# Kernel tuning notes

Hardware: AMD Instinct MI355X
Metric: run time of the kernel (lower is better)

The kernel has to match this reference:

```python
import jax, jax.numpy as jnp
import numpy as np

B, S, D, H, HD = 2, 2048, 1024, 16, 64
DFF = 4 * D
EPS = 1e-6


def _rms(x, w):
    return w * (x * jax.lax.rsqrt(jnp.mean(x * x, axis=-1, keepdims=True) + EPS))


def _rope(x, rope):
    # x: [B, H, S, HD], rope: [S, HD, 2]
    cos = rope[..., 0][None, None]
    sin = rope[..., 1][None, None]
    xr = x.reshape(*x.shape[:-1], -1, 2)
    rot = jnp.stack([-xr[..., 1], xr[..., 0]], axis=-1).reshape(x.shape)
    return x * cos + rot * sin


def setup_inputs() -> dict:
    key = jax.random.key(0)
    ks = jax.random.split(key, 10)
    w = lambda k, shape: jax.random.normal(k, shape, jnp.float32) * 0.02
    return {
        "hidden_states": jax.random.normal(ks[0], (B, S, D), jnp.float32),
        "timestep": jax.random.normal(ks[1], (B, D), jnp.float32),
        "rope_pos_embed": jax.random.normal(ks[2], (S, HD, 2), jnp.float32),
        "adaln_w": w(ks[3], (6 * D, D)),
        "adaln_b": jnp.zeros((6 * D,), jnp.float32),
        "wq": w(ks[4], (D, D)),
        "wk": w(ks[5], (D, D)),
        "wv": w(ks[6], (D, D)),
        "wo": w(ks[7], (D, D)),
        "q_norm_w": jnp.ones((D,), jnp.float32),
        "k_norm_w": jnp.ones((D,), jnp.float32),
        "norm3_w": jnp.ones((D,), jnp.float32),
        "fc1_w": w(ks[8], (DFF, D)),
        "fc1_b": jnp.zeros((DFF,), jnp.float32),
        "fc2_w": w(ks[9], (D, DFF)),
        "fc2_b": jnp.zeros((D,), jnp.float32),
    }


def reference(hidden_states, timestep, rope_pos_embed, adaln_w, adaln_b,
              wq, wk, wv, wo, q_norm_w, k_norm_w, norm3_w,
              fc1_w, fc1_b, fc2_w, fc2_b):
    x = hidden_states  # [B, S, D]
    # AdaLayerNorm: emb = Linear(SiLU(timestep)) -> 6 modulation chunks, broadcast over seq
    emb = jax.nn.silu(timestep) @ adaln_w.T + adaln_b  # [B, 6D]
    sh_msa, sc_msa, g_msa, sh_mlp, sc_mlp, g_mlp = jnp.split(emb[:, None, :], 6, axis=-1)
    mu = jnp.mean(x, axis=-1, keepdims=True)
    var = jnp.mean((x - mu) ** 2, axis=-1, keepdims=True)
    ln = (x - mu) * jax.lax.rsqrt(var + EPS)
    xm = ln * (1.0 + sc_msa) + sh_msa  # modulated input to attention

    # Attention: projections + RMSNorm over inner_dim + RoPE + SDPA
    q = _rms(xm @ wq.T, q_norm_w)
    k = _rms(xm @ wk.T, k_norm_w)
    v = xm @ wv.T
    q = q.reshape(B, S, H, HD).transpose(0, 2, 1, 3)
    k = k.reshape(B, S, H, HD).transpose(0, 2, 1, 3)
    v = v.reshape(B, S, H, HD).transpose(0, 2, 1, 3)
    q = _rope(q, rope_pos_embed)
    k = _rope(k, rope_pos_embed)
    scores = jnp.einsum('bhqd,bhkd->bhqk', q, k) * (HD ** -0.5)
    attn = jax.nn.softmax(scores, axis=-1)
    o = jnp.einsum('bhqk,bhkd->bhqd', attn, v)
    o = o.transpose(0, 2, 1, 3).reshape(B, S, H * HD) @ wo.T

    h = x + g_msa * o  # gated residual

    # MLP branch with AdaLN scale/shift on RMSNorm output
    n3 = _rms(h, norm3_w)
    nm = n3 * (1.0 + sc_mlp) + sh_mlp
    ff = jax.nn.gelu(nm @ fc1_w.T + fc1_b, approximate=True) @ fc2_w.T + fc2_b
    return h + g_mlp * ff
```

## Files before the change

kernel.cpp:

```cpp
#include <hip/hip_runtime.h>
#include <cstdint>
#include <cstddef>

typedef unsigned short ushort_t;
typedef __attribute__((ext_vector_type(8))) short s8v;
typedef __attribute__((ext_vector_type(4))) short s4v;
typedef __attribute__((ext_vector_type(4))) float f4v;

#define MFMA16(a, b, c) __builtin_amdgcn_mfma_f32_16x16x32_bf16(a, b, c, 0, 0, 0)

__device__ __forceinline__ ushort_t f2bf(float f) {
  union { float f; unsigned u; } a; a.f = f;
  return (ushort_t)((a.u + 0x7fffu + ((a.u >> 16) & 1u)) >> 16);
}
__device__ __forceinline__ float bf2f(ushort_t h) {
  union { unsigned u; float f; } a; a.u = ((unsigned)h) << 16; return a.f;
}
__device__ __forceinline__ unsigned fbits(float f) {
  union { float f; unsigned u; } a; a.f = f; return a.u;
}

__device__ __forceinline__ void gload16(const void* g, void* l) {
  __builtin_amdgcn_global_load_lds(
      (__attribute__((address_space(1))) void*)(uintptr_t)g,
      (__attribute__((address_space(3))) void*)(unsigned)(uintptr_t)l,
      16, 0, 0);
}

__launch_bounds__(256)
__global__ void convert_w(const float* __restrict__ wq, const float* __restrict__ wk,
                          const float* __restrict__ wv, const float* __restrict__ wo,
                          const float* __restrict__ f1, const float* __restrict__ f2,
                          ushort_t* __restrict__ dqkv, ushort_t* __restrict__ dwo,
                          ushort_t* __restrict__ df1, ushort_t* __restrict__ df2)
{
  const int blk = blockIdx.x;
  const float* src; ushort_t* dst; int off;
  if      (blk < 1024) { src = wq; dst = dqkv;            off = blk; }
  else if (blk < 2048) { src = wk; dst = dqkv + 1048576;  off = blk - 1024; }
  else if (blk < 3072) { src = wv; dst = dqkv + 2097152;  off = blk - 2048; }
  else if (blk < 4096) { src = wo; dst = dwo;             off = blk - 3072; }
  else if (blk < 8192) { src = f1; dst = df1;             off = blk - 4096; }
  else                 { src = f2; dst = df2;             off = blk - 8192; }
  const int idx = off * 1024 + threadIdx.x * 4;
  float4 v = *(const float4*)(src + idx);
  s4v o;
  o[0] = (short)f2bf(v.x); o[1] = (short)f2bf(v.y);
  o[2] = (short)f2bf(v.z); o[3] = (short)f2bf(v.w);
  *(s4v*)(dst + idx) = o;
}

__launch_bounds__(256)
__global__ void adaln(const float* __restrict__ ts, const float* __restrict__ w,
                      const float* __restrict__ bias, float* __restrict__ emb)
{
  const int j = blockIdx.x * 4 + (threadIdx.x >> 6);
  const int lane = threadIdx.x & 63;
  const float* wr = w + (size_t)j * 1024;
  float s0 = 0.f, s1 = 0.f;
  for (int i = lane; i < 1024; i += 64) {
    const float wv = wr[i];
    const float t0 = ts[i], t1 = ts[1024 + i];
    const float e0 = __builtin_amdgcn_exp2f(-1.4426950409f * t0);
    const float e1 = __builtin_amdgcn_exp2f(-1.4426950409f * t1);
    s0 += wv * t0 * __builtin_amdgcn_rcpf(1.f + e0);
    s1 += wv * t1 * __builtin_amdgcn_rcpf(1.f + e1);
  }
  #pragma unroll
  for (int m = 32; m; m >>= 1) { s0 += __shfl_down(s0, m); s1 += __shfl_down(s1, m); }
  if (!lane) { emb[j] = s0 + bias[j]; emb[6144 + j] = s1 + bias[j]; }
}

__launch_bounds__(256)
__global__ void ln_mod(const float* __restrict__ x, const float* __restrict__ emb,
                       ushort_t* __restrict__ xm)
{
  const int row = blockIdx.x, b = row >> 11, tid = threadIdx.x;
  const float* xr = x + (size_t)row * 1024;
  const int c = tid * 4;
  float4 v = *(const float4*)(xr + c);
  float s  = v.x + v.y + v.z + v.w;
  float s2 = v.x*v.x + v.y*v.y + v.z*v.z + v.w*v.w;
  #pragma unroll
  for (int m = 32; m; m >>= 1) { s += __shfl_down(s, m); s2 += __shfl_down(s2, m); }
  __shared__ float red[8];
  const int wave = tid >> 6, lane = tid & 63;
  if (!lane) { red[wave] = s; red[4 + wave] = s2; }
  __syncthreads();
  const float mu = (red[0] + red[1] + red[2] + red[3]) * (1.f / 1024.f);
  const float ms = (red[4] + red[5] + red[6] + red[7]) * (1.f / 1024.f);
  const float rstd = rsqrtf(ms - mu * mu + 1e-6f);
  const float* sh = emb + b * 6144;
  const float* sc = emb + b * 6144 + 1024;
  float4 shv = *(const float4*)(sh + c);
  float4 scv = *(const float4*)(sc + c);
  s4v ov;
  ov[0] = (short)f2bf((v.x - mu) * rstd * (1.f + scv.x) + shv.x);
  ov[1] = (short)f2bf((v.y - mu) * rstd * (1.f + scv.y) + shv.y);
  ov[2] = (short)f2bf((v.z - mu) * rstd * (1.f + scv.z) + shv.z);
  ov[3] = (short)f2bf((v.w - mu) * rstd * (1.f + scv.w) + shv.w);
  *(s4v*)(xm + (size_t)row * 1024 + c) = ov;
}

template<int EPI, int TN>
__launch_bounds__(256, 4)
__global__ void gemm_bt(const ushort_t* __restrict__ A, const ushort_t* __restrict__ Bw,
                        int K, int N,
                        ushort_t* __restrict__ outb, float* __restrict__ outf,
                        const float* __restrict__ bias, const float* __restrict__ resid,
                        const float* __restrict__ emb, int gate_off)
{
  constexpr int JN = TN / 32;
  constexpr int BUFB = TN * 32;
  __shared__ ushort_t As0[128 * 32], As1[128 * 32];
  __shared__ ushort_t Bs0[BUFB],    Bs1[BUFB];
  const int tid = threadIdx.x;
  const int wave = tid >> 6, lane = tid & 63;
  const int quad = lane >> 4, r = lane & 15;
  const int m0 = blockIdx.y * 128, n0 = blockIdx.x * TN;
  const int wm = (wave >> 1) * 64, wn = (wave & 1) * (TN / 2);

  const int srow = wave * 16 + (lane >> 2);
  const int scol = (lane & 3) * 8;
  const ushort_t* ag = A  + (size_t)(m0 + srow) * K + scol;
  const ushort_t* bg = Bw + (size_t)(n0 + srow) * K + scol;
  const size_t rowK64 = (size_t)64 * K;

  f4v acc[4][JN] = {};

  auto stage = [&](ushort_t* as, ushort_t* bs) {
    gload16(ag,          as + wave * 512);
    gload16(ag + rowK64, as + wave * 512 + 2048);
    gload16(bg,          bs + wave * 512);
    if (TN == 128) gload16(bg + rowK64, bs + wave * 512 + 2048);
    ag += 32; bg += 32;
  };
  auto compute = [&](const ushort_t* ab, const ushort_t* bb) {
    s8v af[4], bf[JN];
    #pragma unroll
    for (int i = 0; i < 4; i++)
      af[i] = *(const s8v*)(ab + (wm + i * 16 + r) * 32 + quad * 8);
    #pragma unroll
    for (int j = 0; j < JN; j++)
      bf[j] = *(const s8v*)(bb + (wn + j * 16 + r) * 32 + quad * 8);
    #pragma unroll
    for (int i = 0; i < 4; i++)
      #pragma unroll
      for (int j = 0; j < JN; j++)
        acc[i][j] = MFMA16(af[i], bf[j], acc[i][j]);
  };

  stage(As0, Bs0);
  __syncthreads();
  const int R = (K >> 6) - 1;
  for (int it = 0; it < R; it++) {
    stage(As1, Bs1);
    compute(As0, Bs0);
    __syncthreads();
    stage(As0, Bs0);
    compute(As1, Bs1);
    __syncthreads();
  }
  stage(As1, Bs1);
  compute(As0, Bs0);
  __syncthreads();
  compute(As1, Bs1);

  const int bblk = m0 >> 11;
  float bj[JN], gj[JN];
  #pragma unroll
  for (int j = 0; j < JN; j++) {
    const int col = n0 + wn + j * 16 + r;
    bj[j] = (EPI == 2 || EPI == 3) ? bias[col] : 0.f;
    gj[j] = (EPI == 1 || EPI == 3) ? emb[bblk * 6144 + gate_off + col] : 0.f;
  }
  #pragma unroll
  for (int i = 0; i < 4; i++) {
    #pragma unroll
    for (int rr = 0; rr < 4; rr++) {
      const int row = m0 + wm + i * 16 + quad * 4 + rr;
      const size_t rbase = (size_t)row * N + n0 + wn;
      #pragma unroll
      for (int j = 0; j < JN; j++) {
        float v = acc[i][j][rr];
        const size_t idx = rbase + j * 16 + r;
        if (EPI == 0) {
          outb[idx] = f2bf(v);
        } else if (EPI == 1) {
          outf[idx] = resid[idx] + gj[j] * v;
        } else if (EPI == 2) {
          v += bj[j];
          const float t = fmaf(v * v, 0.1029436f, 2.3022083f);
          const float e = __builtin_amdgcn_exp2f(-v * t);
          outb[idx] = f2bf(v * __builtin_amdgcn_rcpf(1.f + e));
        } else {
          outf[idx] = resid[idx] + gj[j] * (v + bj[j]);
        }
      }
    }
  }
}

#define G8_PHASE(AB, BB, KS, MH, LOADB)                                       \
  {                                                                           \
    s8v af[4];                                                                \
    const int ck = ((((KS) << 2) | quad) ^ rx) << 3;                          \
    const ushort_t* Ap = (AB) + (wm + (MH) * 64 + r) * 64 + ck;               \
    af[0] = *(const s8v*)(Ap);                                                \
    af[1] = *(const s8v*)(Ap + 1024);                                         \
    af[2] = *(const s8v*)(Ap + 2048);                                         \
    af[3] = *(const s8v*)(Ap + 3072);                                         \
    if (LOADB) {                                                              \
      const ushort_t* Bp = (BB) + (wn + r) * 64 + ck;                         \
      bf[0] = *(const s8v*)(Bp);                                              \
      bf[1] = *(const s8v*)(Bp + 1024);                                       \
      bf[2] = *(const s8v*)(Bp + 2048);                                       \
      bf[3] = *(const s8v*)(Bp + 3072);                                       \
    }                                                                         \
    __builtin_amdgcn_s_barrier();                                             \
    __builtin_amdgcn_s_setprio(1);                                            \
    _Pragma("unroll")                                                         \
    for (int i_ = 0; i_ < 4; i_++) {                                          \
      _Pragma("unroll")                                                       \
      for (int j_ = 0; j_ < 4; j_++)                                          \
        acc[(MH) * 4 + i_][j_] = MFMA16(af[i_], bf[j_], acc[(MH) * 4 + i_][j_]); \
    }                                                                         \
    __builtin_amdgcn_s_setprio(0);                                            \
    __builtin_amdgcn_s_barrier();                                             \
  }

template<int EPI>
__launch_bounds__(512, 2)
__global__ void gemm8p(const ushort_t* __restrict__ A, const ushort_t* __restrict__ Bw,
                       int K, int N, ushort_t* __restrict__ outb,
                       const float* __restrict__ bias)
{
  __shared__ ushort_t Ash[2][256 * 64];
  __shared__ ushort_t Bsh[2][256 * 64];
  const int tid = threadIdx.x;
  const int wid = tid >> 6, lane = tid & 63;
  const int quad = lane >> 4, r = lane & 15, rx = r & 7;

  const int nwg = gridDim.x * gridDim.y;
  int wg = blockIdx.y * gridDim.x + blockIdx.x;
  wg = (wg & 7) * (nwg >> 3) + (wg >> 3);
  const int bx = wg % gridDim.x, by = wg / gridDim.x;
  const int m0 = by * 256, n0 = bx * 256;
  const int wm = (wid >> 2) * 128;
  const int wn = (wid & 3) * 64;

  const int srow = lane >> 3;
  const int scol = ((lane & 7) ^ srow) * 8;
  const ushort_t* ag = A  + (size_t)(m0 + wid * 32 + srow) * K + scol;
  const ushort_t* bg = Bw + (size_t)(n0 + wid * 32 + srow) * K + scol;
  const size_t row8K = (size_t)8 * K;

  f4v acc[8][4] = {};

  auto STAGE = [&](int buf, int kt) {
    const size_t ko = (size_t)kt * 64;
    ushort_t* Ad = &Ash[buf][wid * 2048];
    ushort_t* Bd = &Bsh[buf][wid * 2048];
    #pragma unroll
    for (int c = 0; c < 4; c++)
      gload16(ag + ko + c * row8K, Ad + c * 512);
    #pragma unroll
    for (int c = 0; c < 4; c++)
      gload16(bg + ko + c * row8K, Bd + c * 512);
  };

  STAGE(0, 0);
  STAGE(1, 1);
  asm volatile("s_waitcnt vmcnt(8)" ::: "memory");
  __builtin_amdgcn_s_barrier();

  const int NT = K >> 6;
  #pragma unroll 1
  for (int t = 0; t < NT; t += 2) {
    {
      const ushort_t* Ab = &Ash[0][0];
      const ushort_t* Bb = &Bsh[0][0];
      s8v bf[4];
      G8_PHASE(Ab, Bb, 0, 0, true);
      G8_PHASE(Ab, Bb, 0, 1, false);
      G8_PHASE(Ab, Bb, 1, 0, true);
      G8_PHASE(Ab, Bb, 1, 1, false);
      if (t + 2 < NT) {
        STAGE(0, t + 2);
        asm volatile("s_waitcnt vmcnt(8)" ::: "memory");
      } else {
        asm volatile("s_waitcnt vmcnt(0)" ::: "memory");
      }
      __builtin_amdgcn_s_barrier();
    }
    {
      const ushort_t* Ab = &Ash[1][0];
      const ushort_t* Bb = &Bsh[1][0];
      s8v bf[4];
      G8_PHASE(Ab, Bb, 0, 0, true);
      G8_PHASE(Ab, Bb, 0, 1, false);
      G8_PHASE(Ab, Bb, 1, 0, true);
      G8_PHASE(Ab, Bb, 1, 1, false);
      if (t + 3 < NT) {
        STAGE(1, t + 3);
        asm volatile("s_waitcnt vmcnt(8)" ::: "memory");
      } else {
        asm volatile("s_waitcnt vmcnt(0)" ::: "memory");
      }
      __builtin_amdgcn_s_barrier();
    }
  }

  float bj[4];
  #pragma unroll
  for (int j = 0; j < 4; j++)
    bj[j] = (EPI == 2) ? bias[n0 + wn + j * 16 + r] : 0.f;
  #pragma unroll
  for (int i = 0; i < 8; i++) {
    #pragma unroll
    for (int rr = 0; rr < 4; rr++) {
      const int row = m0 + wm + i * 16 + quad * 4 + rr;
      const size_t rbase = (size_t)row * N + n0 + wn;
      #pragma unroll
      for (int j = 0; j < 4; j++) {
        float v = acc[i][j][rr];
        const size_t idx = rbase + j * 16 + r;
        if (EPI == 0) {
          outb[idx] = f2bf(v);
        } else {
          v += bj[j];
          const float tt = fmaf(v * v, 0.1029436f, 2.3022083f);
          const float e = __builtin_amdgcn_exp2f(-v * tt);
          outb[idx] = f2bf(v * __builtin_amdgcn_rcpf(1.f + e));
        }
      }
    }
  }
}

__launch_bounds__(256)
__global__ void qkv_post(const ushort_t* __restrict__ qkv, const float* __restrict__ rope,
                         const float* __restrict__ qw, const float* __restrict__ kw,
                         ushort_t* __restrict__ q_r, ushort_t* __restrict__ k_r,
                         ushort_t* __restrict__ v_r)
{
  const int row = blockIdx.x, b = row >> 11, s = row & 2047, tid = threadIdx.x;
  const ushort_t* base = qkv + (size_t)row * 3072;
  const int c = tid * 4;
  s4v qv = *(const s4v*)(base + c);
  s4v kv = *(const s4v*)(base + 1024 + c);
  s4v vv = *(const s4v*)(base + 2048 + c);
  float qf[4], kf[4]; float sq = 0.f, sk = 0.f;
  #pragma unroll
  for (int i = 0; i < 4; i++) {
    qf[i] = bf2f((ushort_t)qv[i]); kf[i] = bf2f((ushort_t)kv[i]);
    sq += qf[i] * qf[i]; sk += kf[i] * kf[i];
  }
  #pragma unroll
  for (int m = 32; m; m >>= 1) { sq += __shfl_down(sq, m); sk += __shfl_down(sk, m); }
  __shared__ float red[8];
  const int wave = tid >> 6, lane = tid & 63;
  if (!lane) { red[wave] = sq; red[4 + wave] = sk; }
  __syncthreads();
  const float rq = rsqrtf((red[0]+red[1]+red[2]+red[3]) * (1.f/1024.f) + 1e-6f)
                   * 0.18033688011112042f;
  const float rk = rsqrtf((red[4]+red[5]+red[6]+red[7]) * (1.f/1024.f) + 1e-6f);

  const int h = c >> 6, d = c & 63;
  const float* rp = rope + ((size_t)s * 64 + d) * 2;
  float4 r01 = *(const float4*)(rp);
  float4 r23 = *(const float4*)(rp + 4);
  const float q0 = qf[0]*rq*qw[c], q1 = qf[1]*rq*qw[c+1];
  const float q2 = qf[2]*rq*qw[c+2], q3 = qf[3]*rq*qw[c+3];
  const float k0 = kf[0]*rk*kw[c], k1 = kf[1]*rk*kw[c+1];
  const float k2 = kf[2]*rk*kw[c+2], k3 = kf[3]*rk*kw[c+3];
  s4v qo, ko;
  qo[0] = (short)f2bf(q0 * r01.x - q1 * r01.y);
  qo[1] = (short)f2bf(q1 * r01.z + q0 * r01.w);
  qo[2] = (short)f2bf(q2 * r23.x - q3 * r23.y);
  qo[3] = (short)f2bf(q3 * r23.z + q2 * r23.w);
  ko[0] = (short)f2bf(k0 * r01.x - k1 * r01.y);
  ko[1] = (short)f2bf(k1 * r01.z + k0 * r01.w);
  ko[2] = (short)f2bf(k2 * r23.x - k3 * r23.y);
  ko[3] = (short)f2bf(k3 * r23.z + k2 * r23.w);
  const size_t rowbase = ((size_t)(b * 16 + h) * 2048 + s) * 64;
  const int d_s = (((d >> 3) ^ (s & 7)) << 3) | (d & 7);
  *(s4v*)(q_r + rowbase + d) = qo;
  *(s4v*)(k_r + rowbase + d_s) = ko;
  *(s4v*)(v_r + rowbase + d) = vv;
}

__launch_bounds__(256)
__global__ void vtrans(const ushort_t* __restrict__ v_r, ushort_t* __restrict__ v_t)
{
  const int bh = blockIdx.x >> 5, st = blockIdx.x & 31;
  const int s0 = st * 64;
  __shared__ ushort_t tile[64 * 72];
  const int tid = threadIdx.x;
  #pragma unroll
  for (int rep = 0; rep < 2; rep++) {
    const int idx = rep * 256 + tid;
    const int sr = idx >> 3, dc = (idx & 7) << 3;
    s8v val = *(const s8v*)(v_r + ((size_t)bh * 2048 + s0 + sr) * 64 + dc);
    *(s8v*)(tile + sr * 72 + dc) = val;
  }
  __syncthreads();
  #pragma unroll
  for (int rep = 0; rep < 2; rep++) {
    const int idx = rep * 256 + tid;
    const int d = idx >> 3;
    const int scs = (((idx & 7) ^ (d & 7)) << 3);
    s8v val;
    const int sc = (idx & 7) << 3;
    #pragma unroll
    for (int j = 0; j < 8; j++) val[j] = (short)tile[(sc + j) * 72 + d];
    *(s8v*)(v_t + ((size_t)bh * 64 + d) * 2048 + s0 + scs) = val;
  }
}

__launch_bounds__(256, 4)
__global__ void flash(const ushort_t* __restrict__ q_r, const ushort_t* __restrict__ k_r,
                      const ushort_t* __restrict__ v_t, ushort_t* __restrict__ attn)
{
  __shared__ ushort_t Ksh[2][64 * 64];
  __shared__ ushort_t Vsh[2][64 * 64];
  __shared__ ushort_t Psh[4][16 * 64];
  const int bh = blockIdx.x >> 5, qb = blockIdx.x & 31;
  const int tid = threadIdx.x, wave = tid >> 6, lane = tid & 63;
  const int quad = lane >> 4, r = lane & 15;
  const int rx = r & 7;
  const int q0 = qb * 64 + wave * 16;
  const size_t bhS = (size_t)bh * 2048;

  s8v aq0 = *(const s8v*)(q_r + (bhS + q0 + r) * 64 + quad * 8);
  s8v aq1 = *(const s8v*)(q_r + (bhS + q0 + r) * 64 + 32 + quad * 8);

  f4v o[4] = {};
  float mi = -1e30f, li = 0.f;

  const ushort_t* kg = k_r + (bhS + wave * 16 + (lane >> 3)) * 64 + (lane & 7) * 8;
  const ushort_t* vg = v_t + ((size_t)bh * 64 + wave * 16 + (lane >> 3)) * 2048
                       + (lane & 7) * 8;
  const int klo = wave * 1024 + lane * 8;
  const int vlo = wave * 1024 + lane * 8;
  ushort_t* pw = &Psh[wave][0];

  auto stage = [&](ushort_t* kbuf, ushort_t* vbuf, int kb) {
    #pragma unroll
    for (int c = 0; c < 2; c++) {
      gload16(kg + (size_t)(kb + c * 8) * 64, kbuf + klo + c * 512);
      gload16(vg + kb + (size_t)(c * 8) * 2048, vbuf + vlo + c * 512);
    }
  };

  auto step = [&](const ushort_t* Kc, const ushort_t* Vc) {
    f4v st[4];
    __builtin_amdgcn_s_setprio(1);
    #pragma unroll
    for (int t = 0; t < 4; t++) {
      const ushort_t* krow = Kc + (t * 16 + r) * 64;
      s8v k0 = *(const s8v*)(krow + ((quad ^ rx) << 3));
      s8v k1 = *(const s8v*)(krow + (((4 + quad) ^ rx) << 3));
      f4v z = {};
      z = MFMA16(k0, aq0, z);
      z = MFMA16(k1, aq1, z);
      st[t] = z;
    }
    __builtin_amdgcn_s_setprio(0);

    float m4[4];
    #pragma unroll
    for (int t = 0; t < 4; t++)
      m4[t] = fmaxf(fmaxf(st[t][0], st[t][1]), fmaxf(st[t][2], st[t][3]));
    float mloc = fmaxf(fmaxf(m4[0], m4[1]), fmaxf(m4[2], m4[3]));
    mloc = fmaxf(mloc, __shfl_xor(mloc, 16));
    mloc = fmaxf(mloc, __shfl_xor(mloc, 32));
    const float mn = fmaxf(mi, mloc);
    const float al = __builtin_amdgcn_exp2f(mi - mn);

    float p[4][4];
    uint2 pk[4];
    #pragma unroll
    for (int t = 0; t < 4; t++) {
      #pragma unroll
      for (int rr = 0; rr < 4; rr++)
        p[t][rr] = __builtin_amdgcn_exp2f(st[t][rr] - mn);
      const unsigned u0 = fbits(p[t][0]) + 0x8000u;
      const unsigned u1 = fbits(p[t][1]) + 0x8000u;
      const unsigned u2 = fbits(p[t][2]) + 0x8000u;
      const unsigned u3 = fbits(p[t][3]) + 0x8000u;
      pk[t].x = __builtin_amdgcn_perm(u1, u0, 0x07060302u);
      pk[t].y = __builtin_amdgcn_perm(u3, u2, 0x07060302u);
    }

    #pragma unroll
    for (int t = 0; t < 4; t++) {
      const int cw = t * 2 + (quad >> 1);
      const int sc = cw ^ rx;
      *(uint2*)(pw + r * 64 + (sc << 3) + (quad & 1) * 4) = pk[t];
    }

    float alo[4];
    #pragma unroll
    for (int rr = 0; rr < 4; rr++) alo[rr] = __shfl(al, quad * 4 + rr);
    #pragma unroll
    for (int nt = 0; nt < 4; nt++)
      #pragma unroll
      for (int rr = 0; rr < 4; rr++) o[nt][rr] *= alo[rr];

    float s4r[4];
    #pragma unroll
    for (int t = 0; t < 4; t++)
      s4r[t] = (p[t][0] + p[t][1]) + (p[t][2] + p[t][3]);
    float ls = (s4r[0] + s4r[1]) + (s4r[2] + s4r[3]);
    ls += __shfl_xor(ls, 16);
    ls += __shfl_xor(ls, 32);
    li = al * li + ls;
    mi = mn;

    asm volatile("s_waitcnt lgkmcnt(0)" ::: "memory");

    __builtin_amdgcn_s_setprio(1);
    #pragma unroll
    for (int kc = 0; kc < 2; kc++) {
      const int c = kc * 4 + quad;
      const int sc = c ^ rx;
      s8v ap = *(const s8v*)(pw + r * 64 + (sc << 3));
      #pragma unroll
      for (int nt = 0; nt < 4; nt++) {
        s8v bv = *(const s8v*)(Vc + (nt * 16 + r) * 64 + (sc << 3));
        o[nt] = MFMA16(ap, bv, o[nt]);
      }
    }
    __builtin_amdgcn_s_setprio(0);
  };

  stage(Ksh[0], Vsh[0], 0);
  __syncthreads();

  #pragma unroll 1
  for (int kb = 0; kb < 2048; kb += 128) {
    stage(Ksh[1], Vsh[1], kb + 64);
    step(Ksh[0], Vsh[0]);
    __syncthreads();
    if (kb + 128 < 2048) stage(Ksh[0], Vsh[0], kb + 128);
    step(Ksh[1], Vsh[1]);
    __syncthreads();
  }

  const int h = bh & 15, b = bh >> 4;
  const float linv = 1.f / li;
  #pragma unroll
  for (int rr = 0; rr < 4; rr++) {
    const float inv = __shfl(linv, quad * 4 + rr);
    const size_t orow = ((size_t)(b * 2048 + q0 + quad * 4 + rr)) * 1024 + h * 64;
    #pragma unroll
    for (int nt = 0; nt < 4; nt++)
      attn[orow + nt * 16 + r] = f2bf(o[nt][rr] * inv);
  }
}

__launch_bounds__(256)
__global__ void rms3_mod(const float* __restrict__ h, const float* __restrict__ emb,
                         const float* __restrict__ w3, ushort_t* __restrict__ nm)
{
  const int row = blockIdx.x, b = row >> 11, tid = threadIdx.x;
  const float* hr = h + (size_t)row * 1024;
  const int c = tid * 4;
  float4 v = *(const float4*)(hr + c);
  float s2 = v.x*v.x + v.y*v.y + v.z*v.z + v.w*v.w;
  #pragma unroll
  for (int m = 32; m; m >>= 1) s2 += __shfl_down(s2, m);
  __shared__ float red[4];
  const int wave = tid >> 6, lane = tid & 63;
  if (!lane) red[wave] = s2;
  __syncthreads();
  const float rms = rsqrtf((red[0] + red[1] + red[2] + red[3]) * (1.f / 1024.f) + 1e-6f);
  const float* sh = emb + b * 6144 + 3072;
  const float* sc = emb + b * 6144 + 4096;
  float4 shv = *(const float4*)(sh + c);
  float4 scv = *(const float4*)(sc + c);
  float4 wv  = *(const float4*)(w3 + c);
  s4v ov;
  ov[0] = (short)f2bf(v.x * rms * wv.x * (1.f + scv.x) + shv.x);
  ov[1] = (short)f2bf(v.y * rms * wv.y * (1.f + scv.y) + shv.y);
  ov[2] = (short)f2bf(v.z * rms * wv.z * (1.f + scv.z) + shv.z);
  ov[3] = (short)f2bf(v.w * rms * wv.w * (1.f + scv.w) + shv.w);
  *(s4v*)(nm + (size_t)row * 1024 + c) = ov;
}

extern "C" void kernel_launch(void* const* d_in, const int* in_sizes, int n_in,
                              void* d_out, int out_size, void* d_ws, size_t ws_size,
                              hipStream_t stream)
{
  const float* x    = (const float*)d_in[0];
  const float* ts   = (const float*)d_in[1];
  const float* rope = (const float*)d_in[2];
  const float* adw  = (const float*)d_in[3];
  const float* adb  = (const float*)d_in[4];
  const float* wq   = (const float*)d_in[5];
  const float* wk   = (const float*)d_in[6];
  const float* wv   = (const float*)d_in[7];
  const float* wo   = (const float*)d_in[8];
  const float* qnw  = (const float*)d_in[9];
  const float* knw  = (const float*)d_in[10];
  const float* n3w  = (const float*)d_in[11];
  const float* f1w  = (const float*)d_in[12];
  const float* f1b  = (const float*)d_in[13];
  const float* f2w  = (const float*)d_in[14];
  const float* f2b  = (const float*)d_in[15];

  char* ws = (char*)d_ws;
  ushort_t* WQKV = (ushort_t*)(ws + 0);
  ushort_t* WO   = (ushort_t*)(ws + 6291456);
  ushort_t* F1   = (ushort_t*)(ws + 8388608);
  ushort_t* F2   = (ushort_t*)(ws + 16777216);
  float*    EMB  = (float*)   (ws + 25165824);
  float*    H    = (float*)   (ws + 25214976);
  ushort_t* XM   = (ushort_t*)(ws + 41992192);
  ushort_t* QKV  = (ushort_t*)(ws + 50380800);
  ushort_t* QR   = (ushort_t*)(ws + 75546624);
  ushort_t* KR   = (ushort_t*)(ws + 83935232);
  ushort_t* VR   = (ushort_t*)(ws + 92323840);
  ushort_t* VT   = (ushort_t*)(ws + 100712448);
  ushort_t* ATTN = XM;
  ushort_t* NM   = QKV;
  ushort_t* FF1  = QR;

  convert_w<<<12288, 256, 0, stream>>>(wq, wk, wv, wo, f1w, f2w, WQKV, WO, F1, F2);
  adaln<<<1536, 256, 0, stream>>>(ts, adw, adb, EMB);
  ln_mod<<<4096, 256, 0, stream>>>(x, EMB, XM);
  gemm8p<0><<<dim3(12, 16), 512, 0, stream>>>(XM, WQKV, 1024, 3072, QKV, nullptr);
  qkv_post<<<4096, 256, 0, stream>>>(QKV, rope, qnw, knw, QR, KR, VR);
  vtrans<<<1024, 256, 0, stream>>>(VR, VT);
  flash<<<1024, 256, 0, stream>>>(QR, KR, VT, ATTN);
  gemm_bt<1, 64><<<dim3(16, 32), 256, 0, stream>>>(ATTN, WO, 1024, 1024,
      nullptr, H, nullptr, x, EMB, 2048);
  rms3_mod<<<4096, 256, 0, stream>>>(H, EMB, n3w, NM);
  gemm8p<2><<<dim3(16, 16), 512, 0, stream>>>(NM, F1, 1024, 4096, FF1, f1b);
  gemm_bt<3, 64><<<dim3(16, 32), 256, 0, stream>>>(FF1, F2, 4096, 1024,
      nullptr, (float*)d_out, f2b, H, EMB, 5120);
}
```

Measured before the change: 408.3 us.

## Interleave global prefetch into GEMM phases, swizzle gemm_bt tiles, lazy softmax rescale

```diff
diff --git a/kernel.cpp b/kernel.cpp
--- a/kernel.cpp
+++ b/kernel.cpp
@@ -117,7 +117,12 @@
   const int tid = threadIdx.x;
   const int wave = tid >> 6, lane = tid & 63;
   const int quad = lane >> 4, r = lane & 15;
-  const int m0 = blockIdx.y * 128, n0 = blockIdx.x * TN;
+
+  const int nwg = gridDim.x * gridDim.y;
+  int wg = blockIdx.y * gridDim.x + blockIdx.x;
+  wg = (wg & 7) * (nwg >> 3) + (wg >> 3);
+  const int bx = wg % gridDim.x, by = wg / gridDim.x;
+  const int m0 = by * 128, n0 = bx * TN;
   const int wm = (wave >> 1) * 64, wn = (wave & 1) * (TN / 2);
 
   const int srow = wave * 16 + (lane >> 2);
@@ -201,29 +206,39 @@
   }
 }
 
-#define G8_PHASE(AB, BB, KS, MH, LOADB)                                       \
+#define G8P(AB, BB, SDA, SDB, KO, STG, P)                                     \
   {                                                                           \
-    s8v af[4];                                                                \
-    const int ck = ((((KS) << 2) | quad) ^ rx) << 3;                          \
-    const ushort_t* Ap = (AB) + (wm + (MH) * 64 + r) * 64 + ck;               \
-    af[0] = *(const s8v*)(Ap);                                                \
-    af[1] = *(const s8v*)(Ap + 1024);                                         \
-    af[2] = *(const s8v*)(Ap + 2048);                                         \
-    af[3] = *(const s8v*)(Ap + 3072);                                         \
-    if (LOADB) {                                                              \
-      const ushort_t* Bp = (BB) + (wn + r) * 64 + ck;                         \
-      bf[0] = *(const s8v*)(Bp);                                              \
-      bf[1] = *(const s8v*)(Bp + 1024);                                       \
-      bf[2] = *(const s8v*)(Bp + 2048);                                       \
-      bf[3] = *(const s8v*)(Bp + 3072);                                       \
+    s8v af0k0, af0k1, af1k0, af1k1;                                           \
+    {                                                                         \
+      const ushort_t* Ap0 = (AB) + (size_t)(wm + (2*(P)) * 16 + r) * 64;      \
+      const ushort_t* Ap1 = (AB) + (size_t)(wm + (2*(P)+1) * 16 + r) * 64;    \
+      af0k0 = *(const s8v*)(Ap0 + ((quad ^ rx) << 3));                        \
+      af0k1 = *(const s8v*)(Ap0 + (((4 + quad) ^ rx) << 3));                  \
+      af1k0 = *(const s8v*)(Ap1 + ((quad ^ rx) << 3));                        \
+      af1k1 = *(const s8v*)(Ap1 + (((4 + quad) ^ rx) << 3));                  \
+    }                                                                         \
+    if ((P) == 0) {                                                           \
+      _Pragma("unroll")                                                       \
+      for (int j_ = 0; j_ < 4; j_++) {                                        \
+        const ushort_t* Bp = (BB) + (size_t)(wn + j_ * 16 + r) * 64;          \
+        bfv[j_][0] = *(const s8v*)(Bp + ((quad ^ rx) << 3));                  \
+        bfv[j_][1] = *(const s8v*)(Bp + (((4 + quad) ^ rx) << 3));            \
+      }                                                                       \
+    }                                                                         \
+    if (STG) {                                                                \
+      gload16(ag + (KO) + (P) * row8K, (SDA) + (P) * 512);                    \
+      gload16(bg + (KO) + (P) * row8K, (SDB) + (P) * 512);                    \
     }                                                                         \
     __builtin_amdgcn_s_barrier();                                             \
+    asm volatile("s_waitcnt lgkmcnt(0)" ::: "memory");                        \
+    __builtin_amdgcn_sched_barrier(0);                                        \
     __builtin_amdgcn_s_setprio(1);                                            \
     _Pragma("unroll")                                                         \
-    for (int i_ = 0; i_ < 4; i_++) {                                          \
-      _Pragma("unroll")                                                       \
-      for (int j_ = 0; j_ < 4; j_++)                                          \
-        acc[(MH) * 4 + i_][j_] = MFMA16(af[i_], bf[j_], acc[(MH) * 4 + i_][j_]); \
+    for (int j_ = 0; j_ < 4; j_++) {                                          \
+      acc[2*(P)][j_]     = MFMA16(af0k0, bfv[j_][0], acc[2*(P)][j_]);         \
+      acc[2*(P)][j_]     = MFMA16(af0k1, bfv[j_][1], acc[2*(P)][j_]);         \
+      acc[2*(P)+1][j_]   = MFMA16(af1k0, bfv[j_][0], acc[2*(P)+1][j_]);       \
+      acc[2*(P)+1][j_]   = MFMA16(af1k1, bfv[j_][1], acc[2*(P)+1][j_]);       \
     }                                                                         \
     __builtin_amdgcn_s_setprio(0);                                            \
     __builtin_amdgcn_s_barrier();                                             \
@@ -255,24 +270,19 @@
   const ushort_t* bg = Bw + (size_t)(n0 + wid * 32 + srow) * K + scol;
   const size_t row8K = (size_t)8 * K;
 
+  ushort_t* A0d = &Ash[0][wid * 2048];
+  ushort_t* B0d = &Bsh[0][wid * 2048];
+  ushort_t* A1d = &Ash[1][wid * 2048];
+  ushort_t* B1d = &Bsh[1][wid * 2048];
+
   f4v acc[8][4] = {};
 
-  auto STAGE = [&](int buf, int kt) {
-    const size_t ko = (size_t)kt * 64;
-    ushort_t* Ad = &Ash[buf][wid * 2048];
-    ushort_t* Bd = &Bsh[buf][wid * 2048];
-    #pragma unroll
-    for (int c = 0; c < 4; c++)
-      gload16(ag + ko + c * row8K, Ad + c * 512);
-    #pragma unroll
-    for (int c = 0; c < 4; c++)
-      gload16(bg + ko + c * row8K, Bd + c * 512);
-  };
-
-  STAGE(0, 0);
-  STAGE(1, 1);
-  asm volatile("s_waitcnt vmcnt(8)" ::: "memory");
-  __builtin_amdgcn_s_barrier();
+  #pragma unroll
+  for (int c = 0; c < 4; c++) {
+    gload16(ag + c * row8K, A0d + c * 512);
+    gload16(bg + c * row8K, B0d + c * 512);
+  }
+  __syncthreads();
 
   const int NT = K >> 6;
   #pragma unroll 1
@@ -280,34 +290,25 @@
     {
       const ushort_t* Ab = &Ash[0][0];
       const ushort_t* Bb = &Bsh[0][0];
-      s8v bf[4];
-      G8_PHASE(Ab, Bb, 0, 0, true);
-      G8_PHASE(Ab, Bb, 0, 1, false);
-      G8_PHASE(Ab, Bb, 1, 0, true);
-      G8_PHASE(Ab, Bb, 1, 1, false);
-      if (t + 2 < NT) {
-        STAGE(0, t + 2);
-        asm volatile("s_waitcnt vmcnt(8)" ::: "memory");
-      } else {
-        asm volatile("s_waitcnt vmcnt(0)" ::: "memory");
-      }
-      __builtin_amdgcn_s_barrier();
+      const size_t ko = (size_t)(t + 1) * 64;
+      s8v bfv[4][2];
+      G8P(Ab, Bb, A1d, B1d, ko, true, 0);
+      G8P(Ab, Bb, A1d, B1d, ko, true, 1);
+      G8P(Ab, Bb, A1d, B1d, ko, true, 2);
+      G8P(Ab, Bb, A1d, B1d, ko, true, 3);
+      __syncthreads();
     }
     {
       const ushort_t* Ab = &Ash[1][0];
       const ushort_t* Bb = &Bsh[1][0];
-      s8v bf[4];
-      G8_PHASE(Ab, Bb, 0, 0, true);
-      G8_PHASE(Ab, Bb, 0, 1, false);
-      G8_PHASE(Ab, Bb, 1, 0, true);
-      G8_PHASE(Ab, Bb, 1, 1, false);
-      if (t + 3 < NT) {
-        STAGE(1, t + 3);
-        asm volatile("s_waitcnt vmcnt(8)" ::: "memory");
-      } else {
-        asm volatile("s_waitcnt vmcnt(0)" ::: "memory");
-      }
-      __builtin_amdgcn_s_barrier();
+      const size_t ko = (size_t)(t + 2) * 64;
+      const bool stg = (t + 2) < NT;
+      s8v bfv[4][2];
+      G8P(Ab, Bb, A0d, B0d, ko, stg, 0);
+      G8P(Ab, Bb, A0d, B0d, ko, stg, 1);
+      G8P(Ab, Bb, A0d, B0d, ko, stg, 2);
+      G8P(Ab, Bb, A0d, B0d, ko, stg, 3);
+      __syncthreads();
     }
   }
 
@@ -475,8 +476,9 @@
     float mloc = fmaxf(fmaxf(m4[0], m4[1]), fmaxf(m4[2], m4[3]));
     mloc = fmaxf(mloc, __shfl_xor(mloc, 16));
     mloc = fmaxf(mloc, __shfl_xor(mloc, 32));
-    const float mn = fmaxf(mi, mloc);
-    const float al = __builtin_amdgcn_exp2f(mi - mn);
+
+    const bool grow = !__all(mloc - mi <= 8.f);
+    const float mref = grow ? fmaxf(mi, mloc) : mi;
 
     float p[4][4];
     uint2 pk[4];
@@ -484,7 +486,7 @@
     for (int t = 0; t < 4; t++) {
       #pragma unroll
       for (int rr = 0; rr < 4; rr++)
-        p[t][rr] = __builtin_amdgcn_exp2f(st[t][rr] - mn);
+        p[t][rr] = __builtin_amdgcn_exp2f(st[t][rr] - mref);
       const unsigned u0 = fbits(p[t][0]) + 0x8000u;
       const unsigned u1 = fbits(p[t][1]) + 0x8000u;
       const unsigned u2 = fbits(p[t][2]) + 0x8000u;
@@ -500,13 +502,18 @@
       *(uint2*)(pw + r * 64 + (sc << 3) + (quad & 1) * 4) = pk[t];
     }
 
-    float alo[4];
-    #pragma unroll
-    for (int rr = 0; rr < 4; rr++) alo[rr] = __shfl(al, quad * 4 + rr);
-    #pragma unroll
-    for (int nt = 0; nt < 4; nt++)
+    if (grow) {
+      const float al = __builtin_amdgcn_exp2f(mi - mref);
+      float alo[4];
       #pragma unroll
-      for (int rr = 0; rr < 4; rr++) o[nt][rr] *= alo[rr];
+      for (int rr = 0; rr < 4; rr++) alo[rr] = __shfl(al, quad * 4 + rr);
+      #pragma unroll
+      for (int nt = 0; nt < 4; nt++)
+        #pragma unroll
+        for (int rr = 0; rr < 4; rr++) o[nt][rr] *= alo[rr];
+      li *= al;
+      mi = mref;
+    }
 
     float s4r[4];
     #pragma unroll
@@ -515,8 +522,7 @@
     float ls = (s4r[0] + s4r[1]) + (s4r[2] + s4r[3]);
     ls += __shfl_xor(ls, 16);
     ls += __shfl_xor(ls, 32);
-    li = al * li + ls;
-    mi = mn;
+    li += ls;
 
     asm volatile("s_waitcnt lgkmcnt(0)" ::: "memory");
 
```

Result: faster. 385.9 us (-5.5%).
